# Optimization experiments

Hardware: AMD Instinct MI355X
Metric: run time of the kernel (lower is better)

Reference implementation:

```python
import jax, jax.numpy as jnp
import numpy as np

NEG_INF = -1e8  # matches neg_inf in the torch source


def setup_inputs() -> dict:
    key = jax.random.key(0)
    k1, k2 = jax.random.split(key)
    N, M = 2048, 2048
    theta = jax.random.normal(k1, (N, M, 3), dtype=jnp.float32)
    A = jax.random.normal(k2, (3, 3), dtype=jnp.float32)
    return {"theta": theta, "A": A}


def _viterbi_forward(theta, A):
    # Softmax-smoothed Viterbi (Needleman-Wunsch-style) DP.
    # States: m=0, x=1, y=2.
    # V[i,j,m] = theta[i-1,j-1,m] + lse(V[i-1,j-1] + A[m])
    # V[i,j,x] = theta[i-1,j-1,x] + lse(V[i-1,j]   + A[x])
    # V[i,j,y] = theta[i-1,j-1,y] + lse(V[i,j-1]   + A[y])
    N, M, _ = theta.shape
    dt = theta.dtype
    ninf = jnp.asarray(NEG_INF, dt)
    Am, Ax, Ay = A[0], A[1], A[2]

    # Row 0 of V (columns 0..M): V[0,0]=[0,-inf,-inf], rest -inf.
    row0 = jnp.full((M + 1, 3), NEG_INF, dtype=dt).at[0, 0].set(0.0)

    def row_step(prev_row, theta_row):
        # prev_row: (M+1, 3) = V[i-1, 0..M]; theta_row: (M, 3) = theta[i-1]
        # m and x states depend only on the previous row -> vectorized over j.
        vm = jax.nn.logsumexp(prev_row[:-1] + Am, axis=-1) + theta_row[:, 0]  # (M,) j=1..M
        vx = jax.nn.logsumexp(prev_row[1:] + Ax, axis=-1) + theta_row[:, 1]   # (M,)
        # y state has a same-row recurrence over j -> scan over columns.
        vm_prev = jnp.concatenate([ninf[None], vm[:-1]])  # V[i, j-1, m]
        vx_prev = jnp.concatenate([ninf[None], vx[:-1]])  # V[i, j-1, x]

        def col_step(vy_prev, inputs):
            vmp, vxp, th_y = inputs
            vy = jax.nn.logsumexp(jnp.stack([vmp, vxp, vy_prev]) + Ay) + th_y
            return vy, vy

        _, vy = jax.lax.scan(col_step, ninf, (vm_prev, vx_prev, theta_row[:, 2]))
        new_row = jnp.concatenate(
            [jnp.full((1, 3), NEG_INF, dtype=dt),  # V[i, 0] = -inf
             jnp.stack([vm, vx, vy], axis=-1)], axis=0)
        return new_row, None

    last_row, _ = jax.lax.scan(row_step, row0, theta)
    # Terminal: Vt = lse(V[N, M])
    return jax.nn.logsumexp(last_row[M])


def reference(theta, A):
    return _viterbi_forward(theta, A)
```

## Files before the change

kernel.cpp:

```cpp
#include <hip/hip_runtime.h>

#define NDIM  2048
#define WAVES 32
#define BCOLS 2176
#define SLOTS 2128
#define ENCB  0x40000000
#define SENTV 0xFFFFFFFFFFFFFFFFull

typedef unsigned long long u64;

__device__ __align__(16) float4 g_S4[(size_t)WAVES * SLOTS * 64];
__device__ __align__(16) u64    g_B[(size_t)(WAVES+1) * BCOLS * 2];

__device__ __forceinline__ u64 ald(const u64* p) {
  return __hip_atomic_load(p, __ATOMIC_RELAXED, __HIP_MEMORY_SCOPE_AGENT);
}
__device__ __forceinline__ void ast(u64* p, u64 v) {
  __hip_atomic_store(p, v, __ATOMIC_RELAXED, __HIP_MEMORY_SCOPE_AGENT);
}
__device__ __forceinline__ float shup1(float x) {
  int v = __builtin_amdgcn_update_dpp(0, __float_as_int(x), 0x138, 0xf, 0xf, false);
  return __int_as_float(v);
}
template <int CTRL>
__device__ __forceinline__ float maxdpp(float m) {
  int v = __builtin_amdgcn_update_dpp(__float_as_int(m), __float_as_int(m),
                                      CTRL, 0xf, 0xf, false);
  return fmaxf(m, __int_as_float(v));
}
__device__ __forceinline__ int imax(int a, int b) { return a > b ? a : b; }

typedef const __attribute__((address_space(1))) void GV;
typedef __attribute__((address_space(3)))       void LV;
__device__ __forceinline__ void gll16(const void* g, void* l) {
  __builtin_amdgcn_global_load_lds((GV*)g, (LV*)l, 16, 0, 0);
}

__global__ void vit_prep_theta(const float* __restrict__ theta) {
  const int tid = blockIdx.x * blockDim.x + threadIdx.x;
  const int stride = gridDim.x * blockDim.x;
  const int total = WAVES * SLOTS * 64;
  for (int i = tid; i < total; i += stride) {
    const int l    = i & 63;
    const int rest = i >> 6;
    const int s    = rest % SLOTS;
    const int w    = rest / SLOTS;
    const int row  = w * 64 + l;
    const int col  = s - l;
    float4 r = make_float4(0.f, 0.f, 0.f, 0.f);
    if (col >= 0 && col < NDIM) {
      const float* tp = theta + ((size_t)row * NDIM + col) * 3;
      r.x = __expf(tp[0]); r.y = __expf(tp[1]); r.z = __expf(tp[2]);
    }
    g_S4[i] = r;
  }
}

__global__ void vit_prep_bnd() {
  const int tid = blockIdx.x * blockDim.x + threadIdx.x;
  const int stride = gridDim.x * blockDim.x;
  const int nb = (WAVES+1) * BCOLS;
  const u64 hi0 = ((u64)(unsigned)ENCB) << 32;
  for (int i = tid; i < nb; i += stride) {
    int w = i / BCOLS;
    int c = i - w * BCOLS;
    u64 lo, hi;
    if (c > NDIM)    { lo = 0ull; hi = hi0; }
    else if (w == 0) { lo = (c == 0) ? (u64)__float_as_uint(1.0f) : 0ull; hi = hi0; }
    else if (c == 0) { lo = 0ull; hi = hi0; }
    else             { lo = SENTV; hi = SENTV; }
    ast(&g_B[(size_t)i*2],   lo);
    ast(&g_B[(size_t)i*2+1], hi);
  }
}

__global__ void __launch_bounds__(64, 1)
__attribute__((amdgpu_waves_per_eu(1, 1)))
vit_main(const float* __restrict__ A, float* __restrict__ out) {
  __shared__ float4 sT[2048];
  const int lane = threadIdx.x;
  const int w    = blockIdx.x;
  const bool isL0 = (lane == 0);
  const int lsel = lane & 15;

  const float a00 = __expf(A[0]), a01 = __expf(A[1]), a02 = __expf(A[2]);
  const float a10 = __expf(A[3]), a11 = __expf(A[4]), a12 = __expf(A[5]);
  const float a20 = __expf(A[6]), a21 = __expf(A[7]), a22 = __expf(A[8]);

  const float4* tb4 = g_S4 + (size_t)w * SLOTS * 64 + lane;
  u64* bin  = g_B + (size_t)w     * BCOLS * 2;
  u64* bout = g_B + (size_t)(w+1) * BCOLS * 2;

  float Mp=0.f,Xp=0.f,Yp=0.f, Mu=0.f,Xu=0.f,Yu=0.f, Mud=0.f,Xud=0.f,Yud=0.f;
  int e_w = 0;

  u64* rpn;
  u64 cLo, cHi;
  {
    u64* rp0 = bin + (size_t)(2 + lsel) * 2;
    cLo = ald(rp0); cHi = ald(rp0 + 1);
    rpn = rp0 + 32;
  }
  #pragma unroll
  for (int u_ = 0; u_ < 16; ++u_)
    gll16(tb4 + (size_t)u_ * 64, &sT[u_ * 64]);

  {
    u64 lo = ald(bin), hi = ald(bin + 1);
    while (lo == SENTV || hi == SENTV) { __builtin_amdgcn_s_sleep(2); lo = ald(bin); hi = ald(bin+1); }
    if (isL0) {
      Mud = __uint_as_float((unsigned)lo);
      Xud = __uint_as_float((unsigned)(lo >> 32));
      Yud = __uint_as_float((unsigned)hi);
    }
  }
  {
    u64 lo = ald(bin + 2), hi = ald(bin + 3);
    while (lo == SENTV || hi == SENTV) { __builtin_amdgcn_s_sleep(8); lo = ald(bin+2); hi = ald(bin+3); }
    int ep = (int)((unsigned)(hi >> 32) - (unsigned)ENCB);
    int dd = ep - e_w;
    if (__builtin_amdgcn_readfirstlane(dd) > 48) { e_w = ep; dd = 0; }
    if (isL0) {
      Mu = ldexpf(__uint_as_float((unsigned)lo), dd);
      Xu = ldexpf(__uint_as_float((unsigned)(lo >> 32)), dd);
      Yu = ldexpf(__uint_as_float((unsigned)hi), dd);
    }
  }

#define STEPC(U, DV, SM, TM)                                                   \
  {                                                                            \
    const int s = base + (U) + 1;            \
    float mn = DV.x * fmaf(a02, Yud, fmaf(a01, Xud, a00*Mud));                 \
    float xn = DV.y * fmaf(a12, Yu,  fmaf(a11, Xu,  a10*Mu));                  \
    float yn = DV.z * fmaf(a22, Yp,  fmaf(a21, Xp,  a20*Mp));                  \
    if ((SM) ? (lane == 63) : (s >= 64 && lane == 63)) {                       \
      u64 slo = ((u64)__float_as_uint(xn) << 32) | __float_as_uint(mn);        \
      u64 shi = ((u64)(unsigned)(e_w + ENCB) << 32) | __float_as_uint(yn);     \
      ast(bO + (size_t)(U)*2,     slo);                                        \
      ast(bO + (size_t)(U)*2 + 1, shi);                                        \
    }                                                                          \
    if ((TM) && s == 2111 && w == 31 && lane == 63) {                          \
      out[0] = (log2f(mn + xn + yn) + (float)e_w) * 0.69314718055994531f;      \
    }                                                                          \
        \
    const float rM = __int_as_float(__builtin_amdgcn_readlane(__float_as_int(Mbf), (U))); \
    const float rX = __int_as_float(__builtin_amdgcn_readlane(__float_as_int(Xbf), (U))); \
    const float rY = __int_as_float(__builtin_amdgcn_readlane(__float_as_int(Ybf), (U))); \
                                                                   \
    Mud = Mu; Xud = Xu; Yud = Yu;                                              \
    const float sm = shup1(mn);                                                \
    const float sx = shup1(xn);                                                \
    const float sy = shup1(yn);                                                \
    Mu = isL0 ? rM : sm;                                                       \
    Xu = isL0 ? rX : sx;                                                       \
    Yu = isL0 ? rY : sy;                                                       \
    Mp = mn; Xp = xn; Yp = yn;                                                 \
  }
#define STEPR(U, DV, SM, TM) STEPC(U, DV, SM, TM) DV = sT[ldsA + ((U)+4)*64 + lane];

#define BLOCK(SM, TM)                                                          \
  {                                                                            \
    const unsigned ldsA = ((unsigned)(base >> 4) & 1u) << 10;                  \
    const unsigned ldsB = ldsA ^ 1024u;                                        \
            \
    u64* rpc_ = rpn - 32;                                                      \
    bool bad_ = (cLo == SENTV) || (cHi == SENTV);                              \
    while (__ballot(bad_)) {                                                   \
      __builtin_amdgcn_s_sleep(1);                                             \
      cLo = ald(rpc_); cHi = ald(rpc_ + 1);                                    \
      bad_ = (cLo == SENTV) || (cHi == SENTV);                                 \
    }                                                                          \
        \
    __builtin_amdgcn_s_waitcnt(0x0F70);                     \
    __builtin_amdgcn_sched_barrier(0);                                         \
              \
    u64 nLo = ald(rpn), nHi = ald(rpn + 1);                                    \
    rpn += 32;                                                                 \
    {                                                                          \
      const float4* tn_ = tb4 + (size_t)(base + 16) * 64;                      \
      _Pragma("unroll")                                                        \
      for (int u_ = 0; u_ < 16; ++u_)                                          \
        gll16(tn_ + (size_t)u_ * 64, &sT[ldsB + u_ * 64]);                     \
    }                                                                          \
    __builtin_amdgcn_sched_barrier(0);                                         \
             \
    int dsl = ((int)(unsigned)(cHi >> 32) - ENCB) - e_w;                       \
    if (__ballot(dsl > 0)) {                              \
      int dm = dsl;                                                            \
      dm = imax(dm, __shfl_xor(dm, 1));                                        \
      dm = imax(dm, __shfl_xor(dm, 2));                                        \
      dm = imax(dm, __shfl_xor(dm, 4));                                        \
      dm = imax(dm, __shfl_xor(dm, 8));                                        \
      const int sh = -dm;                                                      \
      Mp = ldexpf(Mp,sh); Xp = ldexpf(Xp,sh); Yp = ldexpf(Yp,sh);              \
      Mu = ldexpf(Mu,sh); Xu = ldexpf(Xu,sh); Yu = ldexpf(Yu,sh);              \
      Mud= ldexpf(Mud,sh);Xud= ldexpf(Xud,sh);Yud= ldexpf(Yud,sh);             \
      e_w += dm; dsl -= dm;                                                    \
    }                                                                          \
    const float Mbf = ldexpf(__uint_as_float((unsigned)cLo), dsl);             \
    const float Xbf = ldexpf(__uint_as_float((unsigned)(cLo >> 32)), dsl);     \
    const float Ybf = ldexpf(__uint_as_float((unsigned)cHi), dsl);             \
                                \
    float4 d0 = sT[ldsA + 0*64 + lane];                                        \
    float4 d1 = sT[ldsA + 1*64 + lane];                                        \
    float4 d2 = sT[ldsA + 2*64 + lane];                                        \
    float4 d3 = sT[ldsA + 3*64 + lane];                                        \
                                                       \
    u64* bO = bout + (size_t)(base - 62) * 2;                                  \
    STEPR(0, d0, SM, TM)  STEPR(1, d1, SM, TM)                                 \
    STEPR(2, d2, SM, TM)  STEPR(3, d3, SM, TM)                                 \
    STEPR(4, d0, SM, TM)  STEPR(5, d1, SM, TM)                                 \
    STEPR(6, d2, SM, TM)  STEPR(7, d3, SM, TM)                                 \
    STEPR(8, d0, SM, TM)  STEPR(9, d1, SM, TM)                                 \
    STEPR(10, d2, SM, TM) STEPR(11, d3, SM, TM)                                \
    STEPC(12, d0, SM, TM) STEPC(13, d1, SM, TM)                                \
    STEPC(14, d2, SM, TM) STEPC(15, d3, SM, TM)                                \
                    \
    {                                                                          \
      float m = fmaxf(fmaxf(Mp, Xp), Yp);                                      \
      const int jl = base + 16 - lane;                                         \
      if (jl < 1 || jl > NDIM) m = 0.0f;                                       \
      m = maxdpp<0x111>(m);                                    \
      m = maxdpp<0x112>(m);                                    \
      m = maxdpp<0x114>(m);                                    \
      m = maxdpp<0x118>(m);                                    \
      m = maxdpp<0x142>(m);                                  \
      m = maxdpp<0x143>(m);            \
      const int mb = __builtin_amdgcn_readlane(__float_as_int(m), 63);         \
      int E = ((mb >> 23) & 0xFF) - 127;                                       \
      if (mb == 0) E = 0;                                                      \
      const int sh = -E;                                                       \
      Mp = ldexpf(Mp,sh); Xp = ldexpf(Xp,sh); Yp = ldexpf(Yp,sh);              \
      Mu = ldexpf(Mu,sh); Xu = ldexpf(Xu,sh); Yu = ldexpf(Yu,sh);              \
      Mud= ldexpf(Mud,sh);Xud= ldexpf(Xud,sh);Yud= ldexpf(Yud,sh);             \
      e_w += E;                                                                \
    }                                                                          \
    base += 16; cLo = nLo; cHi = nHi;                                          \
  }

  int base = 0;
  BLOCK(0, 0) BLOCK(0, 0) BLOCK(0, 0) BLOCK(0, 0)
  for (int it = 0; it < 127; ++it) { BLOCK(1, 0) }
  BLOCK(1, 1)
#undef BLOCK
#undef STEPR
#undef STEPC
}

extern "C" void kernel_launch(void* const* d_in, const int* in_sizes, int n_in,
                              void* d_out, int out_size, void* d_ws, size_t ws_size,
                              hipStream_t stream) {
  const float* theta = (const float*)d_in[0];
  const float* A     = (const float*)d_in[1];
  float* out = (float*)d_out;
  (void)in_sizes; (void)n_in; (void)out_size; (void)d_ws; (void)ws_size;
  vit_prep_theta<<<dim3(8192), dim3(256), 0, stream>>>(theta);
  vit_prep_bnd<<<dim3(256), dim3(256), 0, stream>>>();
  vit_main<<<dim3(WAVES), dim3(64), 0, stream>>>(A, out);
}
```

Measured before the change: 732.9 us.

## Shrink block to 12 steps, preload theta tile, batch boundary stores via LDS

Reduces the per-block step count from 16 to 12, loads all 12 theta float4 values from LDS at the start of each block, and pins them in registers with an empty asm barrier. Boundary values are staged in a small LDS buffer and written out once per block by 12 lanes instead of lane 63 storing each step. The sentinel check now tests each 32-bit half separately, and the prefetch of the next tile is issued after the boundary wait. The intent is to shorten the inter-wave dependency latency and reduce store serialization on the critical path, at the cost of more blocks and changed wait/prefetch ordering.

```diff
diff --git a/kernel.cpp b/kernel.cpp
--- a/kernel.cpp
+++ b/kernel.cpp
@@ -74,14 +74,20 @@
   }
 }
 
+__device__ __forceinline__ bool isbad(u64 lo, u64 hi) {
+  return ((unsigned)lo == 0xFFFFFFFFu) || ((unsigned)(lo >> 32) == 0xFFFFFFFFu) ||
+         ((unsigned)hi == 0xFFFFFFFFu) || ((unsigned)(hi >> 32) == 0xFFFFFFFFu);
+}
+
 __global__ void __launch_bounds__(64, 1)
 __attribute__((amdgpu_waves_per_eu(1, 1)))
 vit_main(const float* __restrict__ A, float* __restrict__ out) {
-  __shared__ float4 sT[2048];
+  __shared__ float4 sT[1536];
+  __shared__ float4 sB[12];
   const int lane = threadIdx.x;
   const int w    = blockIdx.x;
   const bool isL0 = (lane == 0);
-  const int lsel = lane & 15;
+  const int li   = lane % 12;
 
   const float a00 = __expf(A[0]), a01 = __expf(A[1]), a02 = __expf(A[2]);
   const float a10 = __expf(A[3]), a11 = __expf(A[4]), a12 = __expf(A[5]);
@@ -97,17 +103,17 @@
   u64* rpn;
   u64 cLo, cHi;
   {
-    u64* rp0 = bin + (size_t)(2 + lsel) * 2;
+    u64* rp0 = bin + (size_t)(2 + li) * 2;
     cLo = ald(rp0); cHi = ald(rp0 + 1);
-    rpn = rp0 + 32;
+    rpn = rp0 + 24;
   }
   #pragma unroll
-  for (int u_ = 0; u_ < 16; ++u_)
+  for (int u_ = 0; u_ < 12; ++u_)
     gll16(tb4 + (size_t)u_ * 64, &sT[u_ * 64]);
 
   {
     u64 lo = ald(bin), hi = ald(bin + 1);
-    while (lo == SENTV || hi == SENTV) { __builtin_amdgcn_s_sleep(2); lo = ald(bin); hi = ald(bin+1); }
+    while (isbad(lo, hi)) { __builtin_amdgcn_s_sleep(2); lo = ald(bin); hi = ald(bin+1); }
     if (isL0) {
       Mud = __uint_as_float((unsigned)lo);
       Xud = __uint_as_float((unsigned)(lo >> 32));
@@ -116,7 +122,7 @@
   }
   {
     u64 lo = ald(bin + 2), hi = ald(bin + 3);
-    while (lo == SENTV || hi == SENTV) { __builtin_amdgcn_s_sleep(8); lo = ald(bin+2); hi = ald(bin+3); }
+    while (isbad(lo, hi)) { __builtin_amdgcn_s_sleep(8); lo = ald(bin+2); hi = ald(bin+3); }
     int ep = (int)((unsigned)(hi >> 32) - (unsigned)ENCB);
     int dd = ep - e_w;
     if (__builtin_amdgcn_readfirstlane(dd) > 48) { e_w = ep; dd = 0; }
@@ -127,26 +133,22 @@
     }
   }
 
-#define STEPC(U, DV, SM, TM)                                                   \
+  unsigned ldsA = 0;
+
+#define STEP(U, TM)                                                            \
   {                                                                            \
     const int s = base + (U) + 1;            \
-    float mn = DV.x * fmaf(a02, Yud, fmaf(a01, Xud, a00*Mud));                 \
-    float xn = DV.y * fmaf(a12, Yu,  fmaf(a11, Xu,  a10*Mu));                  \
-    float yn = DV.z * fmaf(a22, Yp,  fmaf(a21, Xp,  a20*Mp));                  \
-    if ((SM) ? (lane == 63) : (s >= 64 && lane == 63)) {                       \
-      u64 slo = ((u64)__float_as_uint(xn) << 32) | __float_as_uint(mn);        \
-      u64 shi = ((u64)(unsigned)(e_w + ENCB) << 32) | __float_as_uint(yn);     \
-      ast(bO + (size_t)(U)*2,     slo);                                        \
-      ast(bO + (size_t)(U)*2 + 1, shi);                                        \
-    }                                                                          \
+    float mn = t##U.x * fmaf(a02, Yud, fmaf(a01, Xud, a00*Mud));               \
+    float xn = t##U.y * fmaf(a12, Yu,  fmaf(a11, Xu,  a10*Mu));                \
+    float yn = t##U.z * fmaf(a22, Yp,  fmaf(a21, Xp,  a20*Mp));                \
+    if (lane == 63)                                                            \
+      sB[U] = make_float4(mn, xn, yn, __int_as_float(e_w + ENCB));             \
     if ((TM) && s == 2111 && w == 31 && lane == 63) {                          \
       out[0] = (log2f(mn + xn + yn) + (float)e_w) * 0.69314718055994531f;      \
     }                                                                          \
-        \
     const float rM = __int_as_float(__builtin_amdgcn_readlane(__float_as_int(Mbf), (U))); \
     const float rX = __int_as_float(__builtin_amdgcn_readlane(__float_as_int(Xbf), (U))); \
     const float rY = __int_as_float(__builtin_amdgcn_readlane(__float_as_int(Ybf), (U))); \
-                                                                   \
     Mud = Mu; Xud = Xu; Yud = Yu;                                              \
     const float sm = shup1(mn);                                                \
     const float sx = shup1(xn);                                                \
@@ -156,33 +158,41 @@
     Yu = isL0 ? rY : sy;                                                       \
     Mp = mn; Xp = xn; Yp = yn;                                                 \
   }
-#define STEPR(U, DV, SM, TM) STEPC(U, DV, SM, TM) DV = sT[ldsA + ((U)+4)*64 + lane];
-
-#define BLOCK(SM, TM)                                                          \
+
+#define BLOCK(TM)                                                              \
   {                                                                            \
-    const unsigned ldsA = ((unsigned)(base >> 4) & 1u) << 10;                  \
-    const unsigned ldsB = ldsA ^ 1024u;                                        \
             \
-    u64* rpc_ = rpn - 32;                                                      \
-    bool bad_ = (cLo == SENTV) || (cHi == SENTV);                              \
+    __builtin_amdgcn_s_waitcnt(0x0F72);                          \
+    __builtin_amdgcn_sched_barrier(0);                                         \
+        \
+    float4 t0  = sT[ldsA + 0*64  + lane], t1  = sT[ldsA + 1*64  + lane];       \
+    float4 t2  = sT[ldsA + 2*64  + lane], t3  = sT[ldsA + 3*64  + lane];       \
+    float4 t4  = sT[ldsA + 4*64  + lane], t5  = sT[ldsA + 5*64  + lane];       \
+    float4 t6  = sT[ldsA + 6*64  + lane], t7  = sT[ldsA + 7*64  + lane];       \
+    float4 t8  = sT[ldsA + 8*64  + lane], t9  = sT[ldsA + 9*64  + lane];       \
+    float4 t10 = sT[ldsA + 10*64 + lane], t11 = sT[ldsA + 11*64 + lane];       \
+    asm volatile(""                                                            \
+      : "+v"(t0.x),  "+v"(t0.y),  "+v"(t0.z),                                  \
+        "+v"(t1.x),  "+v"(t1.y),  "+v"(t1.z),                                  \
+        "+v"(t2.x),  "+v"(t2.y),  "+v"(t2.z),                                  \
+        "+v"(t3.x),  "+v"(t3.y),  "+v"(t3.z),                                  \
+        "+v"(t4.x),  "+v"(t4.y),  "+v"(t4.z),                                  \
+        "+v"(t5.x),  "+v"(t5.y),  "+v"(t5.z),                                  \
+        "+v"(t6.x),  "+v"(t6.y),  "+v"(t6.z),                                  \
+        "+v"(t7.x),  "+v"(t7.y),  "+v"(t7.z),                                  \
+        "+v"(t8.x),  "+v"(t8.y),  "+v"(t8.z),                                  \
+        "+v"(t9.x),  "+v"(t9.y),  "+v"(t9.z),                                  \
+        "+v"(t10.x), "+v"(t10.y), "+v"(t10.z),                                 \
+        "+v"(t11.x), "+v"(t11.y), "+v"(t11.z),                                 \
+        "+v"(cLo),   "+v"(cHi));                                               \
+      \
+    u64* rpc_ = rpn - 24;                                                      \
+    bool bad_ = isbad(cLo, cHi);                                               \
     while (__ballot(bad_)) {                                                   \
       __builtin_amdgcn_s_sleep(1);                                             \
       cLo = ald(rpc_); cHi = ald(rpc_ + 1);                                    \
-      bad_ = (cLo == SENTV) || (cHi == SENTV);                                 \
-    }                                                                          \
-        \
-    __builtin_amdgcn_s_waitcnt(0x0F70);                     \
-    __builtin_amdgcn_sched_barrier(0);                                         \
-              \
-    u64 nLo = ald(rpn), nHi = ald(rpn + 1);                                    \
-    rpn += 32;                                                                 \
-    {                                                                          \
-      const float4* tn_ = tb4 + (size_t)(base + 16) * 64;                      \
-      _Pragma("unroll")                                                        \
-      for (int u_ = 0; u_ < 16; ++u_)                                          \
-        gll16(tn_ + (size_t)u_ * 64, &sT[ldsB + u_ * 64]);                     \
-    }                                                                          \
-    __builtin_amdgcn_sched_barrier(0);                                         \
+      bad_ = isbad(cLo, cHi);                                                  \
+    }                                                                          \
              \
     int dsl = ((int)(unsigned)(cHi >> 32) - ENCB) - e_w;                       \
     if (__ballot(dsl > 0)) {                              \
@@ -200,25 +210,36 @@
     const float Mbf = ldexpf(__uint_as_float((unsigned)cLo), dsl);             \
     const float Xbf = ldexpf(__uint_as_float((unsigned)(cLo >> 32)), dsl);     \
     const float Ybf = ldexpf(__uint_as_float((unsigned)cHi), dsl);             \
-                                \
-    float4 d0 = sT[ldsA + 0*64 + lane];                                        \
-    float4 d1 = sT[ldsA + 1*64 + lane];                                        \
-    float4 d2 = sT[ldsA + 2*64 + lane];                                        \
-    float4 d3 = sT[ldsA + 3*64 + lane];                                        \
-                                                       \
-    u64* bO = bout + (size_t)(base - 62) * 2;                                  \
-    STEPR(0, d0, SM, TM)  STEPR(1, d1, SM, TM)                                 \
-    STEPR(2, d2, SM, TM)  STEPR(3, d3, SM, TM)                                 \
-    STEPR(4, d0, SM, TM)  STEPR(5, d1, SM, TM)                                 \
-    STEPR(6, d2, SM, TM)  STEPR(7, d3, SM, TM)                                 \
-    STEPR(8, d0, SM, TM)  STEPR(9, d1, SM, TM)                                 \
-    STEPR(10, d2, SM, TM) STEPR(11, d3, SM, TM)                                \
-    STEPC(12, d0, SM, TM) STEPC(13, d1, SM, TM)                                \
-    STEPC(14, d2, SM, TM) STEPC(15, d3, SM, TM)                                \
+         \
+    u64 nLo = ald(rpn), nHi = ald(rpn + 1);                                    \
+    rpn += 24;                                                                 \
+    {                                                                          \
+      const float4* tn_ = tb4 + (size_t)(base + 12) * 64;                      \
+      _Pragma("unroll")                                                        \
+      for (int u_ = 0; u_ < 12; ++u_)                                          \
+        gll16(tn_ + (size_t)u_ * 64, &sT[(ldsA ^ 768u) + u_ * 64]);            \
+    }                                                                          \
+    __builtin_amdgcn_sched_barrier(0);                                         \
+                                          \
+    STEP(0, TM)  STEP(1, TM)  STEP(2, TM)  STEP(3, TM)                         \
+    STEP(4, TM)  STEP(5, TM)  STEP(6, TM)  STEP(7, TM)                         \
+    STEP(8, TM)  STEP(9, TM)  STEP(10, TM) STEP(11, TM)                        \
+              \
+    {                                                                          \
+      const int col_ = base - 62 + lane;                                       \
+      if (lane < 12 && col_ >= 1) {                                            \
+        float4 v = sB[lane];                                                   \
+        u64 lo_ = ((u64)__float_as_uint(v.y) << 32) | __float_as_uint(v.x);    \
+        u64 hi_ = ((u64)__float_as_uint(v.w) << 32) | __float_as_uint(v.z);    \
+        u64* bO_ = bout + (size_t)col_ * 2;                                    \
+        ast(bO_,     lo_);                                                     \
+        ast(bO_ + 1, hi_);                                                     \
+      }                                                                        \
+    }                                                                          \
                     \
     {                                                                          \
       float m = fmaxf(fmaxf(Mp, Xp), Yp);                                      \
-      const int jl = base + 16 - lane;                                         \
+      const int jl = base + 12 - lane;                                         \
       if (jl < 1 || jl > NDIM) m = 0.0f;                                       \
       m = maxdpp<0x111>(m);                                    \
       m = maxdpp<0x112>(m);                                    \
@@ -235,16 +256,14 @@
       Mud= ldexpf(Mud,sh);Xud= ldexpf(Xud,sh);Yud= ldexpf(Yud,sh);             \
       e_w += E;                                                                \
     }                                                                          \
-    base += 16; cLo = nLo; cHi = nHi;                                          \
+    base += 12; ldsA ^= 768u; cLo = nLo; cHi = nHi;                            \
   }
 
   int base = 0;
-  BLOCK(0, 0) BLOCK(0, 0) BLOCK(0, 0) BLOCK(0, 0)
-  for (int it = 0; it < 127; ++it) { BLOCK(1, 0) }
-  BLOCK(1, 1)
+  for (int it = 0; it < 175; ++it) { BLOCK(0) }
+  BLOCK(1)
 #undef BLOCK
-#undef STEPR
-#undef STEPC
+#undef STEP
 }
 
 extern "C" void kernel_launch(void* const* d_in, const int* in_sizes, int n_in,
```

Result: no change. 743.1 us (+1.4%).

## Triple-buffer theta prefetch and batch boundary stores through LDS

Applied to the files above, without the earlier changes.

Switches the LDS theta staging from double to triple buffering, prefetching two blocks ahead and rotating buffer offsets, so global loads have more time to land before use. Boundary values that lane 63 used to store to global memory once per step are now written to a small LDS staging array and flushed by 16 lanes at once at the end of each block. The sentinel check now tests each 32-bit half, which guards against torn 64-bit reads. In exchange the code uses more LDS, drops the explicit waitcnt before the prefetch, and delays boundary publication to the next wave by up to a block.

```diff
diff --git a/kernel.cpp b/kernel.cpp
--- a/kernel.cpp
+++ b/kernel.cpp
@@ -3,7 +3,7 @@
 #define NDIM  2048
 #define WAVES 32
 #define BCOLS 2176
-#define SLOTS 2128
+#define SLOTS 2160
 #define ENCB  0x40000000
 #define SENTV 0xFFFFFFFFFFFFFFFFull
 
@@ -74,10 +74,16 @@
   }
 }
 
+__device__ __forceinline__ bool isbad(u64 lo, u64 hi) {
+  return ((unsigned)lo == 0xFFFFFFFFu) || ((unsigned)(lo >> 32) == 0xFFFFFFFFu) ||
+         ((unsigned)hi == 0xFFFFFFFFu) || ((unsigned)(hi >> 32) == 0xFFFFFFFFu);
+}
+
 __global__ void __launch_bounds__(64, 1)
 __attribute__((amdgpu_waves_per_eu(1, 1)))
 vit_main(const float* __restrict__ A, float* __restrict__ out) {
-  __shared__ float4 sT[2048];
+  __shared__ float4 sT[3072];
+  __shared__ float4 sB[16];
   const int lane = threadIdx.x;
   const int w    = blockIdx.x;
   const bool isL0 = (lane == 0);
@@ -104,10 +110,13 @@
   #pragma unroll
   for (int u_ = 0; u_ < 16; ++u_)
     gll16(tb4 + (size_t)u_ * 64, &sT[u_ * 64]);
+  #pragma unroll
+  for (int u_ = 0; u_ < 16; ++u_)
+    gll16(tb4 + (size_t)(16 + u_) * 64, &sT[1024 + u_ * 64]);
 
   {
     u64 lo = ald(bin), hi = ald(bin + 1);
-    while (lo == SENTV || hi == SENTV) { __builtin_amdgcn_s_sleep(2); lo = ald(bin); hi = ald(bin+1); }
+    while (isbad(lo, hi)) { __builtin_amdgcn_s_sleep(2); lo = ald(bin); hi = ald(bin+1); }
     if (isL0) {
       Mud = __uint_as_float((unsigned)lo);
       Xud = __uint_as_float((unsigned)(lo >> 32));
@@ -116,7 +125,7 @@
   }
   {
     u64 lo = ald(bin + 2), hi = ald(bin + 3);
-    while (lo == SENTV || hi == SENTV) { __builtin_amdgcn_s_sleep(8); lo = ald(bin+2); hi = ald(bin+3); }
+    while (isbad(lo, hi)) { __builtin_amdgcn_s_sleep(8); lo = ald(bin+2); hi = ald(bin+3); }
     int ep = (int)((unsigned)(hi >> 32) - (unsigned)ENCB);
     int dd = ep - e_w;
     if (__builtin_amdgcn_readfirstlane(dd) > 48) { e_w = ep; dd = 0; }
@@ -126,19 +135,19 @@
       Yu = ldexpf(__uint_as_float((unsigned)hi), dd);
     }
   }
-
-#define STEPC(U, DV, SM, TM)                                                   \
+  __builtin_amdgcn_sched_barrier(0);
+
+  unsigned cur = 0, nx1 = 1024, nx2 = 2048;
+
+#define STEPC(U, DV, TM)                                                       \
   {                                                                            \
     const int s = base + (U) + 1;            \
     float mn = DV.x * fmaf(a02, Yud, fmaf(a01, Xud, a00*Mud));                 \
     float xn = DV.y * fmaf(a12, Yu,  fmaf(a11, Xu,  a10*Mu));                  \
     float yn = DV.z * fmaf(a22, Yp,  fmaf(a21, Xp,  a20*Mp));                  \
-    if ((SM) ? (lane == 63) : (s >= 64 && lane == 63)) {                       \
-      u64 slo = ((u64)__float_as_uint(xn) << 32) | __float_as_uint(mn);        \
-      u64 shi = ((u64)(unsigned)(e_w + ENCB) << 32) | __float_as_uint(yn);     \
-      ast(bO + (size_t)(U)*2,     slo);                                        \
-      ast(bO + (size_t)(U)*2 + 1, shi);                                        \
-    }                                                                          \
+    \
+    if (lane == 63)                                                            \
+      sB[U] = make_float4(mn, xn, yn, __int_as_float(e_w + ENCB));             \
     if ((TM) && s == 2111 && w == 31 && lane == 63) {                          \
       out[0] = (log2f(mn + xn + yn) + (float)e_w) * 0.69314718055994531f;      \
     }                                                                          \
@@ -156,31 +165,17 @@
     Yu = isL0 ? rY : sy;                                                       \
     Mp = mn; Xp = xn; Yp = yn;                                                 \
   }
-#define STEPR(U, DV, SM, TM) STEPC(U, DV, SM, TM) DV = sT[ldsA + ((U)+4)*64 + lane];
-
-#define BLOCK(SM, TM)                                                          \
+#define STEPR(U, DV, TM) STEPC(U, DV, TM) DV = sT[cur + ((U)+4)*64 + lane];
+
+#define BLOCK(TM)                                                              \
   {                                                                            \
-    const unsigned ldsA = ((unsigned)(base >> 4) & 1u) << 10;                  \
-    const unsigned ldsB = ldsA ^ 1024u;                                        \
-            \
+                        \
     u64* rpc_ = rpn - 32;                                                      \
-    bool bad_ = (cLo == SENTV) || (cHi == SENTV);                              \
+    bool bad_ = isbad(cLo, cHi);                                               \
     while (__ballot(bad_)) {                                                   \
       __builtin_amdgcn_s_sleep(1);                                             \
       cLo = ald(rpc_); cHi = ald(rpc_ + 1);                                    \
-      bad_ = (cLo == SENTV) || (cHi == SENTV);                                 \
-    }                                                                          \
-        \
-    __builtin_amdgcn_s_waitcnt(0x0F70);                     \
-    __builtin_amdgcn_sched_barrier(0);                                         \
-              \
-    u64 nLo = ald(rpn), nHi = ald(rpn + 1);                                    \
-    rpn += 32;                                                                 \
-    {                                                                          \
-      const float4* tn_ = tb4 + (size_t)(base + 16) * 64;                      \
-      _Pragma("unroll")                                                        \
-      for (int u_ = 0; u_ < 16; ++u_)                                          \
-        gll16(tn_ + (size_t)u_ * 64, &sT[ldsB + u_ * 64]);                     \
+      bad_ = isbad(cLo, cHi);                                                  \
     }                                                                          \
     __builtin_amdgcn_sched_barrier(0);                                         \
              \
@@ -200,21 +195,39 @@
     const float Mbf = ldexpf(__uint_as_float((unsigned)cLo), dsl);             \
     const float Xbf = ldexpf(__uint_as_float((unsigned)(cLo >> 32)), dsl);     \
     const float Ybf = ldexpf(__uint_as_float((unsigned)cHi), dsl);             \
-                                \
-    float4 d0 = sT[ldsA + 0*64 + lane];                                        \
-    float4 d1 = sT[ldsA + 1*64 + lane];                                        \
-    float4 d2 = sT[ldsA + 2*64 + lane];                                        \
-    float4 d3 = sT[ldsA + 3*64 + lane];                                        \
+                      \
+    u64 nLo = ald(rpn), nHi = ald(rpn + 1);                                    \
+    rpn += 32;                                                                 \
+                          \
+    {                                                                          \
+      const float4* tn_ = tb4 + (size_t)(base + 32) * 64;                      \
+      _Pragma("unroll")                                                        \
+      for (int u_ = 0; u_ < 16; ++u_)                                          \
+        gll16(tn_ + (size_t)u_ * 64, &sT[nx2 + u_ * 64]);                      \
+    }                                                                          \
+    __builtin_amdgcn_sched_barrier(0);                                         \
+            \
+    float4 d0 = sT[cur + 0*64 + lane];                                         \
+    float4 d1 = sT[cur + 1*64 + lane];                                         \
+    float4 d2 = sT[cur + 2*64 + lane];                                         \
+    float4 d3 = sT[cur + 3*64 + lane];                                         \
                                                        \
-    u64* bO = bout + (size_t)(base - 62) * 2;                                  \
-    STEPR(0, d0, SM, TM)  STEPR(1, d1, SM, TM)                                 \
-    STEPR(2, d2, SM, TM)  STEPR(3, d3, SM, TM)                                 \
-    STEPR(4, d0, SM, TM)  STEPR(5, d1, SM, TM)                                 \
-    STEPR(6, d2, SM, TM)  STEPR(7, d3, SM, TM)                                 \
-    STEPR(8, d0, SM, TM)  STEPR(9, d1, SM, TM)                                 \
-    STEPR(10, d2, SM, TM) STEPR(11, d3, SM, TM)                                \
-    STEPC(12, d0, SM, TM) STEPC(13, d1, SM, TM)                                \
-    STEPC(14, d2, SM, TM) STEPC(15, d3, SM, TM)                                \
+    STEPR(0, d0, TM)  STEPR(1, d1, TM)  STEPR(2, d2, TM)  STEPR(3, d3, TM)     \
+    STEPR(4, d0, TM)  STEPR(5, d1, TM)  STEPR(6, d2, TM)  STEPR(7, d3, TM)     \
+    STEPR(8, d0, TM)  STEPR(9, d1, TM)  STEPR(10, d2, TM) STEPR(11, d3, TM)    \
+    STEPC(12, d0, TM) STEPC(13, d1, TM) STEPC(14, d2, TM) STEPC(15, d3, TM)    \
+        \
+    {                                                                          \
+      const int col_ = base - 62 + lane;                                       \
+      if (lane < 16 && col_ >= 1) {                                            \
+        float4 v = sB[lane];                                                   \
+        u64 lo_ = ((u64)__float_as_uint(v.y) << 32) | __float_as_uint(v.x);    \
+        u64 hi_ = ((u64)__float_as_uint(v.w) << 32) | __float_as_uint(v.z);    \
+        u64* bO_ = bout + (size_t)col_ * 2;                                    \
+        ast(bO_,     lo_);                                                     \
+        ast(bO_ + 1, hi_);                                                     \
+      }                                                                        \
+    }                                                                          \
                     \
     {                                                                          \
       float m = fmaxf(fmaxf(Mp, Xp), Yp);                                      \
@@ -235,13 +248,14 @@
       Mud= ldexpf(Mud,sh);Xud= ldexpf(Xud,sh);Yud= ldexpf(Yud,sh);             \
       e_w += E;                                                                \
     }                                                                          \
-    base += 16; cLo = nLo; cHi = nHi;                                          \
+    base += 16;                                                                \
+    { unsigned t_ = cur; cur = nx1; nx1 = nx2; nx2 = t_; }                     \
+    cLo = nLo; cHi = nHi;                                                      \
   }
 
   int base = 0;
-  BLOCK(0, 0) BLOCK(0, 0) BLOCK(0, 0) BLOCK(0, 0)
-  for (int it = 0; it < 127; ++it) { BLOCK(1, 0) }
-  BLOCK(1, 1)
+  for (int it = 0; it < 131; ++it) { BLOCK(0) }
+  BLOCK(1)
 #undef BLOCK
 #undef STEPR
 #undef STEPC
```

Measured after the change: 710.3 us. 1.03x faster.
